# Performance work log

Hardware: AMD Instinct MI355X
Metric: run time of the kernel (lower is better)

## Reference

```python
import jax, jax.numpy as jnp
import numpy as np

VOCAB, EMB_DIM, HIDDEN, NUM_CLASSES = 100000, 128, 256, 20
B, S = 4096, 200


def setup_inputs() -> dict:
    key = jax.random.key(0)
    k1, k2, k3, k4, k5, k6, k7 = jax.random.split(key, 7)
    x = jax.random.randint(k1, (B, S), 0, VOCAB, dtype=jnp.int64)
    seq_lengths = jnp.maximum(jax.random.randint(k2, (B,), 0, S, dtype=jnp.int64), 1)
    emb = jax.random.normal(k3, (VOCAB, EMB_DIM), dtype=jnp.float32) * 0.02
    emb = emb.at[0].set(0.0)  # padding_idx=0
    W1 = jax.random.normal(k4, (EMB_DIM, HIDDEN), dtype=jnp.float32) * (1.0 / np.sqrt(EMB_DIM))
    b1 = jax.random.normal(k5, (HIDDEN,), dtype=jnp.float32) * 0.01
    W2 = jax.random.normal(k6, (HIDDEN, NUM_CLASSES), dtype=jnp.float32) * (1.0 / np.sqrt(HIDDEN))
    b2 = jax.random.normal(k7, (NUM_CLASSES,), dtype=jnp.float32) * 0.01
    return {"x": x, "seq_lengths": seq_lengths, "emb": emb, "W1": W1, "b1": b1, "W2": W2, "b2": b2}


def reference(x, seq_lengths, emb, W1, b1, W2, b2):
    # Embedding lookup: [B, S, D]
    e = emb[x]
    # Masked mean over first seq_lengths[i] positions (fused, no per-sample loop)
    mask = (jnp.arange(S)[None, :] < seq_lengths[:, None]).astype(e.dtype)  # [B, S]
    pooled = jnp.einsum('bsd,bs->bd', e, mask) / seq_lengths[:, None].astype(e.dtype)
    # MLP (dropout is identity in eval mode)
    hidden = jax.nn.relu(pooled @ W1 + b1)
    return hidden @ W2 + b2
```

## Files before the change

kernel.cpp:

```cpp
#include <hip/hip_runtime.h>
#include <hip/hip_bf16.h>

#define B 4096
#define S 200
#define EMB_DIM 128
#define HIDDEN 256
#define NUM_CLASSES 20

__global__ __launch_bounds__(256) void pool_kernel(
    const int* __restrict__ x,
    const int* __restrict__ lens,
    const float* __restrict__ emb,
    float* __restrict__ pooled)
{
    const int b = blockIdx.x;
    const int L = lens[b];
    const int t = threadIdx.x;
    const int g = t >> 5;
    const int d = t & 31;

    const int* xr = x + (long)b * S;

    float4 acc = make_float4(0.f, 0.f, 0.f, 0.f);
    for (int s = g; s < L; s += 8) {
        const int idx = xr[s];
        const float4 v = ((const float4*)(emb + (long)idx * EMB_DIM))[d];
        acc.x += v.x; acc.y += v.y; acc.z += v.z; acc.w += v.w;
    }

    __shared__ float4 tmp[8][32];
    tmp[g][d] = acc;
    __syncthreads();

    if (t < 32) {
        float4 s0 = tmp[0][t];
        #pragma unroll
        for (int gg = 1; gg < 8; ++gg) {
            const float4 v = tmp[gg][t];
            s0.x += v.x; s0.y += v.y; s0.z += v.z; s0.w += v.w;
        }
        const float inv = 1.0f / (float)L;
        s0.x *= inv; s0.y *= inv; s0.z *= inv; s0.w *= inv;
        ((float4*)(pooled + (long)b * EMB_DIM))[t] = s0;
    }
}

#define TB 16
__global__ __launch_bounds__(256) void mlp_kernel(
    const float* __restrict__ pooled,
    const float* __restrict__ W1,
    const float* __restrict__ b1,
    const float* __restrict__ W2,
    const float* __restrict__ b2,
    float* __restrict__ out)
{
    __shared__ float P[TB][EMB_DIM];
    __shared__ float H[TB][HIDDEN];

    const int t = threadIdx.x;
    const int b0 = blockIdx.x * TB;

    for (int i = t; i < TB * EMB_DIM; i += 256) {
        P[i >> 7][i & 127] = pooled[(long)b0 * EMB_DIM + i];
    }
    __syncthreads();

    float acc[TB];
    #pragma unroll
    for (int r = 0; r < TB; ++r) acc[r] = 0.f;

    for (int k = 0; k < EMB_DIM; ++k) {
        const float w = W1[k * HIDDEN + t];
        #pragma unroll
        for (int r = 0; r < TB; ++r) acc[r] += P[r][k] * w;
    }

    const float bb = b1[t];
    #pragma unroll
    for (int r = 0; r < TB; ++r) H[r][t] = fmaxf(acc[r] + bb, 0.f);
    __syncthreads();

    for (int o = t; o < TB * NUM_CLASSES; o += 256) {
        const int r = o / NUM_CLASSES;
        const int c = o - r * NUM_CLASSES;
        float a = b2[c];
        for (int k = 0; k < HIDDEN; ++k) {
            a += H[r][k] * W2[k * NUM_CLASSES + c];
        }
        out[(long)(b0 + r) * NUM_CLASSES + c] = a;
    }
}

extern "C" void kernel_launch(void* const* d_in, const int* in_sizes, int n_in,
                              void* d_out, int out_size, void* d_ws, size_t ws_size,
                              hipStream_t stream) {
    const int*   x    = (const int*)d_in[0];
    const int*   lens = (const int*)d_in[1];
    const float* emb  = (const float*)d_in[2];
    const float* W1   = (const float*)d_in[3];
    const float* b1   = (const float*)d_in[4];
    const float* W2   = (const float*)d_in[5];
    const float* b2   = (const float*)d_in[6];
    float*       out  = (float*)d_out;

    float* pooled = (float*)d_ws;

    pool_kernel<<<B, 256, 0, stream>>>(x, lens, emb, pooled);
    mlp_kernel<<<B / TB, 256, 0, stream>>>(pooled, W1, b1, W2, b2, out);
}
```

Baseline: 150.7 us.

## Stage token indices in LDS, unroll gather by four, shrink MLP batch tile

The pool kernel now loads each sample's token indices into shared memory once and pads them with index 0, whose embedding row is zero. The gather loop then issues four independent embedding loads per iteration into separate accumulators, so more memory requests are in flight. The MLP kernel halves the batch tile to 8 rows, doubling the block count, and reads pooled values from LDS as float4. The output stage now uses one thread per output. Padding with index 0 adds wasted loads of row 0 and relies on that row being zero.

```diff
diff --git a/kernel.cpp b/kernel.cpp
--- a/kernel.cpp
+++ b/kernel.cpp
@@ -3,6 +3,7 @@
 
 #define B 4096
 #define S 200
+#define SPAD 224
 #define EMB_DIM 128
 #define HIDDEN 256
 #define NUM_CLASSES 20
@@ -14,22 +15,46 @@
     float* __restrict__ pooled)
 {
     const int b = blockIdx.x;
+    const int t = threadIdx.x;
     const int L = lens[b];
-    const int t = threadIdx.x;
+
+    __shared__ int sidx[SPAD];
+    __shared__ float4 tmp[8][32];
+
+    if (t < SPAD) {
+        int v = 0;
+        if (t < L) v = x[(long)b * S + t];
+        sidx[t] = v;
+    }
+    __syncthreads();
+
     const int g = t >> 5;
     const int d = t & 31;
 
-    const int* xr = x + (long)b * S;
+    float4 a0 = make_float4(0.f, 0.f, 0.f, 0.f);
+    float4 a1 = a0, a2 = a0, a3 = a0;
 
-    float4 acc = make_float4(0.f, 0.f, 0.f, 0.f);
-    for (int s = g; s < L; s += 8) {
-        const int idx = xr[s];
-        const float4 v = ((const float4*)(emb + (long)idx * EMB_DIM))[d];
-        acc.x += v.x; acc.y += v.y; acc.z += v.z; acc.w += v.w;
+    const int Lpad = (L + 31) & ~31;
+    for (int base = g; base < Lpad; base += 32) {
+        const int i0 = sidx[base];
+        const int i1 = sidx[base + 8];
+        const int i2 = sidx[base + 16];
+        const int i3 = sidx[base + 24];
+        const float4 v0 = ((const float4*)(emb + (long)i0 * EMB_DIM))[d];
+        const float4 v1 = ((const float4*)(emb + (long)i1 * EMB_DIM))[d];
+        const float4 v2 = ((const float4*)(emb + (long)i2 * EMB_DIM))[d];
+        const float4 v3 = ((const float4*)(emb + (long)i3 * EMB_DIM))[d];
+        a0.x += v0.x; a0.y += v0.y; a0.z += v0.z; a0.w += v0.w;
+        a1.x += v1.x; a1.y += v1.y; a1.z += v1.z; a1.w += v1.w;
+        a2.x += v2.x; a2.y += v2.y; a2.z += v2.z; a2.w += v2.w;
+        a3.x += v3.x; a3.y += v3.y; a3.z += v3.z; a3.w += v3.w;
     }
+    a0.x += a1.x + a2.x + a3.x;
+    a0.y += a1.y + a2.y + a3.y;
+    a0.z += a1.z + a2.z + a3.z;
+    a0.w += a1.w + a2.w + a3.w;
 
-    __shared__ float4 tmp[8][32];
-    tmp[g][d] = acc;
+    tmp[g][d] = a0;
     __syncthreads();
 
     if (t < 32) {
@@ -45,7 +70,7 @@
     }
 }
 
-#define TB 16
+#define TB 8
 __global__ __launch_bounds__(256) void mlp_kernel(
     const float* __restrict__ pooled,
     const float* __restrict__ W1,
@@ -69,10 +94,20 @@
     #pragma unroll
     for (int r = 0; r < TB; ++r) acc[r] = 0.f;
 
-    for (int k = 0; k < EMB_DIM; ++k) {
-        const float w = W1[k * HIDDEN + t];
+    for (int k4 = 0; k4 < EMB_DIM; k4 += 4) {
+        float4 p[TB];
         #pragma unroll
-        for (int r = 0; r < TB; ++r) acc[r] += P[r][k] * w;
+        for (int r = 0; r < TB; ++r) p[r] = *(const float4*)&P[r][k4];
+        #pragma unroll
+        for (int kk = 0; kk < 4; ++kk) {
+            const float w = W1[(k4 + kk) * HIDDEN + t];
+            #pragma unroll
+            for (int r = 0; r < TB; ++r) {
+                const float pv = (kk == 0) ? p[r].x : (kk == 1) ? p[r].y
+                               : (kk == 2) ? p[r].z : p[r].w;
+                acc[r] += pv * w;
+            }
+        }
     }
 
     const float bb = b1[t];
@@ -80,9 +115,9 @@
     for (int r = 0; r < TB; ++r) H[r][t] = fmaxf(acc[r] + bb, 0.f);
     __syncthreads();
 
-    for (int o = t; o < TB * NUM_CLASSES; o += 256) {
-        const int r = o / NUM_CLASSES;
-        const int c = o - r * NUM_CLASSES;
+    if (t < TB * NUM_CLASSES) {
+        const int r = t / NUM_CLASSES;
+        const int c = t - r * NUM_CLASSES;
         float a = b2[c];
         for (int k = 0; k < HIDDEN; ++k) {
             a += H[r][k] * W2[k * NUM_CLASSES + c];
```

Result: faster. 135.6 us (-10.0%).

## Fuse pooling and MLP into one per-sample kernel with batched gathers

Applied to the files above, without the earlier changes.

Merges the pooling and MLP kernels into a single kernel with one block per sample, removing the pooled intermediate round-trip and a second launch. Token indices are staged in shared memory, and each thread issues 8 independent embedding-row loads per iteration to raise memory-level parallelism. Positions past the sequence length read row 0, which relies on the padding row being zero. The MLP is no longer batched across samples, so every block re-reads all of W1 and W2 from cache, which adds a lot of L2 traffic.

```diff
diff --git a/kernel.cpp b/kernel.cpp
--- a/kernel.cpp
+++ b/kernel.cpp
@@ -7,29 +7,74 @@
 #define HIDDEN 256
 #define NUM_CLASSES 20
 
-__global__ __launch_bounds__(256) void pool_kernel(
+__global__ __launch_bounds__(256, 4) void fused_kernel(
     const int* __restrict__ x,
     const int* __restrict__ lens,
     const float* __restrict__ emb,
-    float* __restrict__ pooled)
+    const float* __restrict__ W1,
+    const float* __restrict__ b1,
+    const float* __restrict__ W2,
+    const float* __restrict__ b2,
+    float* __restrict__ out)
 {
+    __shared__ int    sidx[256];
+    __shared__ float4 tmp[8][32];
+    __shared__ float  P[EMB_DIM];
+    __shared__ float  H[HIDDEN];
+    __shared__ float  part[8][NUM_CLASSES];
+
     const int b = blockIdx.x;
+    const int t = threadIdx.x;
     const int L = lens[b];
-    const int t = threadIdx.x;
+
+    {
+        int v = 0;
+        if (t < L) v = x[(long)b * S + t];
+        sidx[t] = v;
+    }
+    __syncthreads();
+
     const int g = t >> 5;
     const int d = t & 31;
 
-    const int* xr = x + (long)b * S;
+    const int Lpad  = (L + 63) & ~63;
+    const int nIter = Lpad >> 6;
 
-    float4 acc = make_float4(0.f, 0.f, 0.f, 0.f);
-    for (int s = g; s < L; s += 8) {
-        const int idx = xr[s];
-        const float4 v = ((const float4*)(emb + (long)idx * EMB_DIM))[d];
-        acc.x += v.x; acc.y += v.y; acc.z += v.z; acc.w += v.w;
+    float4 acc[8];
+    #pragma unroll
+    for (int j = 0; j < 8; ++j) acc[j] = make_float4(0.f, 0.f, 0.f, 0.f);
+
+    int cur[8], nxt[8];
+    #pragma unroll
+    for (int j = 0; j < 8; ++j) cur[j] = sidx[g + 8 * j];
+
+    for (int it = 0; it < nIter; ++it) {
+        float4 v[8];
+        #pragma unroll
+        for (int j = 0; j < 8; ++j)
+            v[j] = ((const float4*)(emb + (long)cur[j] * EMB_DIM))[d];
+
+        const int nb = (it + 1) << 6;
+        if (it + 1 < nIter) {
+            #pragma unroll
+            for (int j = 0; j < 8; ++j) nxt[j] = sidx[nb + g + 8 * j];
+        }
+
+        #pragma unroll
+        for (int j = 0; j < 8; ++j) {
+            acc[j].x += v[j].x; acc[j].y += v[j].y;
+            acc[j].z += v[j].z; acc[j].w += v[j].w;
+        }
+        #pragma unroll
+        for (int j = 0; j < 8; ++j) cur[j] = nxt[j];
     }
 
-    __shared__ float4 tmp[8][32];
-    tmp[g][d] = acc;
+    #pragma unroll
+    for (int j = 1; j < 8; ++j) {
+        acc[0].x += acc[j].x; acc[0].y += acc[j].y;
+        acc[0].z += acc[j].z; acc[0].w += acc[j].w;
+    }
+    tmp[g][d] = acc[0];
     __syncthreads();
 
     if (t < 32) {
@@ -41,53 +86,38 @@
         }
         const float inv = 1.0f / (float)L;
         s0.x *= inv; s0.y *= inv; s0.z *= inv; s0.w *= inv;
-        ((float4*)(pooled + (long)b * EMB_DIM))[t] = s0;
-    }
-}
-
-#define TB 16
-__global__ __launch_bounds__(256) void mlp_kernel(
-    const float* __restrict__ pooled,
-    const float* __restrict__ W1,
-    const float* __restrict__ b1,
-    const float* __restrict__ W2,
-    const float* __restrict__ b2,
-    float* __restrict__ out)
-{
-    __shared__ float P[TB][EMB_DIM];
-    __shared__ float H[TB][HIDDEN];
-
-    const int t = threadIdx.x;
-    const int b0 = blockIdx.x * TB;
-
-    for (int i = t; i < TB * EMB_DIM; i += 256) {
-        P[i >> 7][i & 127] = pooled[(long)b0 * EMB_DIM + i];
+        ((float4*)P)[t] = s0;
     }
     __syncthreads();
 
-    float acc[TB];
-    #pragma unroll
-    for (int r = 0; r < TB; ++r) acc[r] = 0.f;
-
-    for (int k = 0; k < EMB_DIM; ++k) {
-        const float w = W1[k * HIDDEN + t];
-        #pragma unroll
-        for (int r = 0; r < TB; ++r) acc[r] += P[r][k] * w;
+    {
+        float h0 = 0.f, h1 = 0.f, h2 = 0.f, h3 = 0.f;
+        for (int k = 0; k < EMB_DIM; k += 4) {
+            h0 += P[k]     * W1[(k)     * HIDDEN + t];
+            h1 += P[k + 1] * W1[(k + 1) * HIDDEN + t];
+            h2 += P[k + 2] * W1[(k + 2) * HIDDEN + t];
+            h3 += P[k + 3] * W1[(k + 3) * HIDDEN + t];
+        }
+        H[t] = fmaxf(h0 + h1 + h2 + h3 + b1[t], 0.f);
     }
-
-    const float bb = b1[t];
-    #pragma unroll
-    for (int r = 0; r < TB; ++r) H[r][t] = fmaxf(acc[r] + bb, 0.f);
     __syncthreads();
 
-    for (int o = t; o < TB * NUM_CLASSES; o += 256) {
-        const int r = o / NUM_CLASSES;
-        const int c = o - r * NUM_CLASSES;
-        float a = b2[c];
-        for (int k = 0; k < HIDDEN; ++k) {
-            a += H[r][k] * W2[k * NUM_CLASSES + c];
-        }
-        out[(long)(b0 + r) * NUM_CLASSES + c] = a;
+    if (t < 8 * NUM_CLASSES) {
+        const int j = t / NUM_CLASSES;
+        const int c = t - j * NUM_CLASSES;
+        const int k0 = j * 32;
+        float a = 0.f;
+        for (int k = k0; k < k0 + 32; ++k)
+            a += H[k] * W2[k * NUM_CLASSES + c];
+        part[j][c] = a;
+    }
+    __syncthreads();
+
+    if (t < NUM_CLASSES) {
+        float a = b2[t];
+        #pragma unroll
+        for (int j = 0; j < 8; ++j) a += part[j][t];
+        out[(long)b * NUM_CLASSES + t] = a;
     }
 }
 
@@ -103,8 +133,5 @@
     const float* b2   = (const float*)d_in[6];
     float*       out  = (float*)d_out;
 
-    float* pooled = (float*)d_ws;
-
-    pool_kernel<<<B, 256, 0, stream>>>(x, lens, emb, pooled);
-    mlp_kernel<<<B / TB, 256, 0, stream>>>(pooled, W1, b1, W2, b2, out);
+    fused_kernel<<<B, 256, 0, stream>>>(x, lens, emb, W1, b1, W2, b2, out);
 }
```

Measured after the change: 126.5 us. 16.0% less time.
